# Kernel tuning notes

Hardware: AMD Instinct MI355X
Metric: run time of the kernel (lower is better)

The kernel has to match this reference:

```python
import jax, jax.numpy as jnp
import numpy as np

EPS = 1e-5

def _ln(x, g, b):
    mu = jnp.mean(x, axis=-1, keepdims=True)
    var = jnp.mean(jnp.square(x - mu), axis=-1, keepdims=True)
    return (x - mu) * jax.lax.rsqrt(var + EPS) * g + b


def setup_inputs() -> dict:
    key = jax.random.key(0)
    ks = jax.random.split(key, 16)
    B, T, D, H = 8, 4096, 512, 1024
    s_d = 1.0 / np.sqrt(D)
    s_h = 1.0 / np.sqrt(H)
    return {
        "x": jax.random.normal(ks[0], (B, T, D), dtype=jnp.float32),
        "gamma": jnp.ones((D,), jnp.float32),
        "beta": jnp.zeros((D,), jnp.float32),
        "Wq": jax.random.uniform(ks[1], (D, H), jnp.float32, -s_d, s_d),
        "bq": jax.random.uniform(ks[2], (H,), jnp.float32, -s_d, s_d),
        "Wk": jax.random.uniform(ks[3], (D, H), jnp.float32, -s_d, s_d),
        "bk": jax.random.uniform(ks[4], (H,), jnp.float32, -s_d, s_d),
        "Wv": jax.random.uniform(ks[5], (D, H), jnp.float32, -s_d, s_d),
        "bv": jax.random.uniform(ks[6], (H,), jnp.float32, -s_d, s_d),
        "wbias": jax.random.uniform(ks[7], (H,), jnp.float32, 0.0, 1.0),
        "Wo": jax.random.uniform(ks[8], (H, D), jnp.float32, -s_h, s_h),
        "bo": jax.random.uniform(ks[9], (D,), jnp.float32, -s_h, s_h),
        "W1": jax.random.uniform(ks[10], (D, H), jnp.float32, -s_d, s_d),
        "b1": jax.random.uniform(ks[11], (H,), jnp.float32, -s_d, s_d),
        "W2": jax.random.uniform(ks[12], (H, D), jnp.float32, -s_h, s_h),
        "b2": jax.random.uniform(ks[13], (D,), jnp.float32, -s_h, s_h),
    }


def reference(x, gamma, beta, Wq, bq, Wk, bk, Wv, bv, wbias, Wo, bo, W1, b1, W2, b2):
    # --- pre-LN ---
    x1 = _ln(x, gamma, beta)                      # [B,T,D]
    # --- AFTFull attention (NOTE: sums over BATCH dim 0, as in original repo) ---
    Q = jnp.einsum('btd,dh->bth', x1, Wq) + bq    # [B,T,H]
    K = jnp.einsum('btd,dh->bth', x1, Wk) + bk
    V = jnp.einsum('btd,dh->bth', x1, Wv) + bv
    Q_sig = jax.nn.sigmoid(Q)
    numer = jnp.exp(K + wbias)                    # [B,T,H]
    denom = jnp.sum(numer, axis=0)                # [T,H]
    weighted = jnp.sum(numer * V, axis=0) / denom # [T,H]
    Yt = Q_sig * weighted                         # [B,T,H] (broadcast)
    Yt = jnp.einsum('bth,hd->btd', Yt, Wo) + bo   # [B,T,D]
    x2 = Yt + x1                                  # residual (dropout = identity, eval)
    # --- second LN (same params, as in original) + MLP ---
    x3 = _ln(x2, gamma, beta)
    h = jax.nn.gelu(jnp.einsum('btd,dh->bth', x3, W1) + b1, approximate=False)
    m = jnp.einsum('bth,hd->btd', h, W2) + b2
    # original: out = dropout(m) + m  ==  2*m at eval (no residual to x2)
    return m + m
```

## Files before the change

kernel.cpp:

```cpp
#include <hip/hip_runtime.h>
#include <hip/hip_bf16.h>
#include <cstdint>

using u16 = unsigned short;
using u32 = unsigned int;

typedef __bf16 bf16x8 __attribute__((ext_vector_type(8)));
typedef float  f32x4  __attribute__((ext_vector_type(4)));

#define DEV static __device__ __forceinline__

DEV float bf2f(u16 u){ union { u32 u; float f; } c; c.u = ((u32)u) << 16; return c.f; }

DEV u16 f2bf(float f){
  __bf16 h = (__bf16)f;
  return __builtin_bit_cast(u16, h);
}

DEV float fast_rcp(float x){ return __builtin_amdgcn_rcpf(x); }

DEV void async16(const u16* g, u16* l){
  __builtin_amdgcn_global_load_lds((const __attribute__((address_space(1))) u32*)g,
                                   (__attribute__((address_space(3))) u32*)l,
                                   16, 0, 0);
}

__global__ __launch_bounds__(256)
void transpose_all(const float* __restrict__ W0, const float* __restrict__ W1,
                   const float* __restrict__ W2, const float* __restrict__ W3,
                   const float* __restrict__ W4, const float* __restrict__ W5,
                   u16* __restrict__ T0, u16* __restrict__ T1, u16* __restrict__ T2,
                   u16* __restrict__ T3, u16* __restrict__ T4, u16* __restrict__ T5){
  const int z = blockIdx.z;
  const float* W; u16* WT; int R, C;
  switch (z){
    case 0:  W = W0; WT = T0; R = 512;  C = 1024; break;
    case 1:  W = W1; WT = T1; R = 512;  C = 1024; break;
    case 2:  W = W2; WT = T2; R = 512;  C = 1024; break;
    case 3:  W = W3; WT = T3; R = 1024; C = 512;  break;
    case 4:  W = W4; WT = T4; R = 512;  C = 1024; break;
    default: W = W5; WT = T5; R = 1024; C = 512;  break;
  }
  const int c0 = blockIdx.x * 32, r0 = blockIdx.y * 32;
  if (c0 >= C || r0 >= R) return;
  __shared__ float tile[32][33];
  const int tx = threadIdx.x, ty = threadIdx.y;
  #pragma unroll
  for (int j = 0; j < 4; ++j)
    tile[ty + j*8][tx] = W[(size_t)(r0 + ty + j*8) * C + (c0 + tx)];
  __syncthreads();
  #pragma unroll
  for (int j = 0; j < 4; ++j)
    WT[(size_t)(c0 + ty + j*8) * R + (r0 + tx)] = f2bf(tile[tx][ty + j*8]);
}

template<bool BF16IN>
__global__ __launch_bounds__(256)
void ln_kernel(const void* __restrict__ xin, const float* __restrict__ gamma,
               const float* __restrict__ beta, u16* __restrict__ xout){
  const int wid = threadIdx.x >> 6;
  const int lane = threadIdx.x & 63;
  const size_t row = (size_t)blockIdx.x * 4 + wid;
  const int d0 = lane * 8;
  float v[8];
  if constexpr (BF16IN){
    const u16* xp = (const u16*)xin + row * 512 + d0;
    uint4 p = *(const uint4*)xp;
    const u16* s = (const u16*)&p;
    #pragma unroll
    for (int i = 0; i < 8; ++i) v[i] = bf2f(s[i]);
  } else {
    const float* xp = (const float*)xin + row * 512 + d0;
    float4 p0 = *(const float4*)xp;
    float4 p1 = *(const float4*)(xp + 4);
    v[0]=p0.x; v[1]=p0.y; v[2]=p0.z; v[3]=p0.w;
    v[4]=p1.x; v[5]=p1.y; v[6]=p1.z; v[7]=p1.w;
  }
  float s = 0.f, sq = 0.f;
  #pragma unroll
  for (int i = 0; i < 8; ++i){ s += v[i]; sq += v[i]*v[i]; }
  #pragma unroll
  for (int o = 32; o >= 1; o >>= 1){ s += __shfl_xor(s, o); sq += __shfl_xor(sq, o); }
  const float mu  = s * (1.0f/512.0f);
  const float var = sq * (1.0f/512.0f) - mu*mu;
  const float rstd = rsqrtf(var + 1e-5f);
  const float4 g0 = *(const float4*)(gamma + d0);
  const float4 g1 = *(const float4*)(gamma + d0 + 4);
  const float4 b0 = *(const float4*)(beta + d0);
  const float4 b1 = *(const float4*)(beta + d0 + 4);
  const float* gp = (const float*)&g0;
  float gg[8] = {g0.x,g0.y,g0.z,g0.w,g1.x,g1.y,g1.z,g1.w};
  float bb[8] = {b0.x,b0.y,b0.z,b0.w,b1.x,b1.y,b1.z,b1.w};
  (void)gp;
  u16 o8[8];
  #pragma unroll
  for (int i = 0; i < 8; ++i)
    o8[i] = f2bf((v[i]-mu)*rstd*gg[i] + bb[i]);
  *(uint4*)(xout + row*512 + d0) = *(const uint4*)o8;
}

__global__ __launch_bounds__(256)
void aft_fused(const u16* __restrict__ numer, const u16* __restrict__ V,
               const u16* __restrict__ qs, u16* __restrict__ yt){
  const size_t TH = (size_t)4096 * 1024;
  const size_t i8 = ((size_t)blockIdx.x * 256 + threadIdx.x) * 8;
  float den[8], ws[8];
  #pragma unroll
  for (int j = 0; j < 8; ++j){ den[j] = 0.f; ws[j] = 0.f; }
  #pragma unroll
  for (int b = 0; b < 8; ++b){
    uint4 pn = *(const uint4*)(numer + b*TH + i8);
    uint4 pv = *(const uint4*)(V     + b*TH + i8);
    const u16* n = (const u16*)&pn;
    const u16* v = (const u16*)&pv;
    #pragma unroll
    for (int j = 0; j < 8; ++j){ float nf = bf2f(n[j]); den[j] += nf; ws[j] += nf * bf2f(v[j]); }
  }
  float w[8];
  #pragma unroll
  for (int j = 0; j < 8; ++j) w[j] = ws[j] * fast_rcp(den[j]);
  #pragma unroll
  for (int b = 0; b < 8; ++b){
    uint4 pq = *(const uint4*)(qs + b*TH + i8);
    const u16* q = (const u16*)&pq;
    u16 o[8];
    #pragma unroll
    for (int j = 0; j < 8; ++j) o[j] = f2bf(bf2f(q[j]) * w[j]);
    *(uint4*)(yt + b*TH + i8) = *(const uint4*)o;
  }
}

template<int EPI, int KC>
__global__ __launch_bounds__(256, 3)
void gemm128(const u16* __restrict__ A, const u16* __restrict__ Bt, int nTiles,
             const float* __restrict__ bias0, const float* __restrict__ wbias,
             u16* __restrict__ out0, u16* __restrict__ out1, u16* __restrict__ out2,
             const float* __restrict__ bias1, const float* __restrict__ bias2,
             const u16* __restrict__ resid, float* __restrict__ outf){
  __shared__ u16 ldsA[128*64];
  __shared__ u16 ldsB[128*64];
  const int tid  = threadIdx.x;
  const int wid  = tid >> 6;
  const int lane = tid & 63;
  const int quad = lane >> 4;
  const int lr   = lane & 15;

  const int lin = blockIdx.x;
  const int GS  = 16 * nTiles;
  const int g   = lin / GS;
  const int rem = lin - g * GS;
  const int tileM = (g * 16 + (rem & 15)) * 128;
  const int tileN = (rem >> 4) * 128;

  const int wmBase = (wid & 1) * 64;
  const int wnBase = (wid >> 1) * 64;

  f32x4 acc[4][4] = {};

  int srow[4], scb[4];
  #pragma unroll
  for (int r = 0; r < 4; ++r){
    const int off = r*4096 + wid*1024 + lane*16;
    srow[r] = off >> 7;
    scb[r]  = ((off >> 4) & 7) ^ (srow[r] & 7);
  }
  const u16* aSrc[4]; const u16* bSrc[4];
  #pragma unroll
  for (int r = 0; r < 4; ++r){
    aSrc[r] = A  + (size_t)(tileM + srow[r]) * KC + scb[r]*8;
    bSrc[r] = Bt + (size_t)(tileN + srow[r]) * KC + scb[r]*8;
  }

  int aOff[2][4], bOff[2][4];
  #pragma unroll
  for (int s = 0; s < 2; ++s)
    #pragma unroll
    for (int i = 0; i < 4; ++i){
      const int m = wmBase + i*16 + lr;
      const int n = wnBase + i*16 + lr;
      aOff[s][i] = m*128 + (((s*4 + quad) ^ (m & 7)) * 16);
      bOff[s][i] = n*128 + (((s*4 + quad) ^ (n & 7)) * 16);
    }

  #pragma unroll
  for (int kt = 0; kt < KC; kt += 64){
    #pragma unroll
    for (int r = 0; r < 4; ++r){
      async16(aSrc[r] + kt, (u16*)((char*)ldsA + r*4096 + wid*1024));
      async16(bSrc[r] + kt, (u16*)((char*)ldsB + r*4096 + wid*1024));
    }
    __syncthreads();
    #pragma unroll
    for (int s = 0; s < 2; ++s){
      bf16x8 ar[4], br[4];
      #pragma unroll
      for (int i = 0; i < 4; ++i) ar[i] = *(const bf16x8*)((const char*)ldsA + aOff[s][i]);
      #pragma unroll
      for (int i = 0; i < 4; ++i) br[i] = *(const bf16x8*)((const char*)ldsB + bOff[s][i]);
      #pragma unroll
      for (int i = 0; i < 4; ++i)
        #pragma unroll
        for (int j = 0; j < 4; ++j)
          acc[i][j] = __builtin_amdgcn_mfma_f32_16x16x32_bf16(br[j], ar[i], acc[i][j], 0, 0, 0);
    }
    __syncthreads();
  }

  if (EPI == 3){
    #pragma unroll
    for (int j = 0; j < 4; ++j){
      const int colb = tileN + wnBase + j*16 + quad*4;
      const float4 bvv = *(const float4*)(bias0 + colb);
      #pragma unroll
      for (int i = 0; i < 4; ++i){
        const int row = tileM + wmBase + i*16 + lr;
        float4 o;
        #pragma unroll
        for (int r = 0; r < 4; ++r)
          ((float*)&o)[r] = 2.0f * (acc[i][j][r] + ((const float*)&bvv)[r]);
        *(float4*)(outf + (size_t)row * 512 + colb) = o;
      }
    }
    return;
  }

  u16* eb = ldsA + wid * 1152;
  const int mat = (EPI == 0) ? (tileN >> 10) : 0;
  const float* biasP = bias0;
  u16* outP = out0;
  int ldO = 1024, cb0 = tileN + wnBase;
  if (EPI == 0){
    biasP = (mat==0) ? bias0 : (mat==1) ? bias1 : bias2;
    outP  = (mat==0) ? out0  : (mat==1) ? out1  : out2;
    cb0   = (tileN & 1023) + wnBase;
  } else if (EPI == 1){
    ldO = 512;
  }

  #pragma unroll
  for (int i = 0; i < 4; ++i){
    const int row = tileM + wmBase + i*16 + lr;
    #pragma unroll
    for (int j = 0; j < 4; ++j){
      const int cl = j*16 + quad*4;
      const float4 bvv = *(const float4*)(biasP + cb0 + cl);
      u16 o[4];
      if (EPI == 0){
        float4 wbv = {0,0,0,0};
        if (mat == 1) wbv = *(const float4*)(wbias + cb0 + cl);
        #pragma unroll
        for (int r = 0; r < 4; ++r){
          float v = acc[i][j][r] + ((const float*)&bvv)[r];
          if (mat == 0)      v = fast_rcp(1.0f + __expf(-v));
          else if (mat == 1) v = __expf(v + ((const float*)&wbv)[r]);
          o[r] = f2bf(v);
        }
      } else if (EPI == 1){
        uint2 pr = *(const uint2*)(resid + (size_t)row * 512 + cb0 + cl);
        const u16* rp = (const u16*)&pr;
        #pragma unroll
        for (int r = 0; r < 4; ++r)
          o[r] = f2bf(acc[i][j][r] + ((const float*)&bvv)[r] + bf2f(rp[r]));
      } else {
        #pragma unroll
        for (int r = 0; r < 4; ++r){
          float v = acc[i][j][r] + ((const float*)&bvv)[r];
          float u2 = 2.0f * v * (0.7978845608f + 0.0356774081f * v * v);
          float t  = 1.0f - 2.0f * fast_rcp(1.0f + __expf(u2));
          o[r] = f2bf(0.5f * v * (1.0f + t));
        }
      }
      *(uint2*)(eb + lr*72 + cl) = *(const uint2*)o;
    }
    __asm__ volatile("s_waitcnt lgkmcnt(0)" ::: "memory");
    uint4 p0 = *(const uint4*)(eb + lr*72 + quad*16);
    uint4 p1 = *(const uint4*)(eb + lr*72 + quad*16 + 8);
    __asm__ volatile("s_waitcnt lgkmcnt(0)" ::: "memory");
    u16* gp = outP + (size_t)row * ldO + cb0 + quad*16;
    *(uint4*)gp = p0;
    *(uint4*)(gp + 8) = p1;
  }
}

extern "C" void kernel_launch(void* const* d_in, const int* in_sizes, int n_in,
                              void* d_out, int out_size, void* d_ws, size_t ws_size,
                              hipStream_t stream) {
  const float* x     = (const float*)d_in[0];
  const float* gamma = (const float*)d_in[1];
  const float* beta  = (const float*)d_in[2];
  const float* Wq    = (const float*)d_in[3];
  const float* bq    = (const float*)d_in[4];
  const float* Wk    = (const float*)d_in[5];
  const float* bk    = (const float*)d_in[6];
  const float* Wv    = (const float*)d_in[7];
  const float* bv    = (const float*)d_in[8];
  const float* wbias = (const float*)d_in[9];
  const float* Wo    = (const float*)d_in[10];
  const float* bo    = (const float*)d_in[11];
  const float* W1    = (const float*)d_in[12];
  const float* b1    = (const float*)d_in[13];
  const float* W2    = (const float*)d_in[14];
  const float* b2    = (const float*)d_in[15];
  float* out = (float*)d_out;

  char* w = (char*)d_ws;
  const size_t MB = 1ull << 20;
  u16* WqkvT = (u16*)(w + 0*MB);
  u16* WoT   = (u16*)(w + 3*MB);
  u16* W1T   = (u16*)(w + 4*MB);
  u16* W2T   = (u16*)(w + 5*MB);
  u16* x1b   = (u16*)(w + 6*MB);
  u16* Qs    = (u16*)(w + 38*MB);
  u16* Nu    = (u16*)(w + 102*MB);
  u16* Vb    = (u16*)(w + 166*MB);
  u16* Yt    = Nu;
  u16* x2b   = Vb;
  u16* x3b   = (u16*)(w + 198*MB);
  u16* hb    = Qs;

  transpose_all<<<dim3(32, 32, 6), dim3(32, 8), 0, stream>>>(
      Wq, Wk, Wv, Wo, W1, W2,
      WqkvT, WqkvT + 1024*512, WqkvT + 2*1024*512, WoT, W1T, W2T);

  ln_kernel<false><<<8192, 256, 0, stream>>>(x, gamma, beta, x1b);

  gemm128<0, 512><<<256*24, 256, 0, stream>>>(x1b, WqkvT, 24,
      bq, wbias, Qs, Nu, Vb, bk, bv, nullptr, nullptr);

  aft_fused<<<2048, 256, 0, stream>>>(Nu, Vb, Qs, Yt);

  gemm128<1, 1024><<<256*4, 256, 0, stream>>>(Yt, WoT, 4,
      bo, nullptr, x2b, nullptr, nullptr, nullptr, nullptr, x1b, nullptr);

  ln_kernel<true><<<8192, 256, 0, stream>>>(x2b, gamma, beta, x3b);

  gemm128<2, 512><<<256*8, 256, 0, stream>>>(x3b, W1T, 8,
      b1, nullptr, hb, nullptr, nullptr, nullptr, nullptr, nullptr, nullptr);

  gemm128<3, 1024><<<256*4, 256, 0, stream>>>(hb, W2T, 4,
      b2, nullptr, nullptr, nullptr, nullptr, nullptr, nullptr, nullptr, out);
}
```

Baseline: 486.7 us.

## Replace 128x128 GEMM with 256x256 ping-pong pipelined 8-wave GEMM

```diff
diff --git a/kernel.cpp b/kernel.cpp
--- a/kernel.cpp
+++ b/kernel.cpp
@@ -24,6 +24,11 @@
                                    (__attribute__((address_space(3))) u32*)l,
                                    16, 0, 0);
 }
+
+#define BARRIER() __builtin_amdgcn_s_barrier()
+#define LGKM0() do { __asm__ volatile("s_waitcnt lgkmcnt(0)" ::: "memory"); \
+                     __builtin_amdgcn_sched_barrier(0); } while (0)
+#define VMCNT(n) __asm__ volatile("s_waitcnt vmcnt(" #n ")" ::: "memory")
 
 __global__ __launch_bounds__(256)
 void transpose_all(const float* __restrict__ W0, const float* __restrict__ W1,
@@ -88,10 +93,8 @@
   const float4 g1 = *(const float4*)(gamma + d0 + 4);
   const float4 b0 = *(const float4*)(beta + d0);
   const float4 b1 = *(const float4*)(beta + d0 + 4);
-  const float* gp = (const float*)&g0;
   float gg[8] = {g0.x,g0.y,g0.z,g0.w,g1.x,g1.y,g1.z,g1.w};
   float bb[8] = {b0.x,b0.y,b0.z,b0.w,b1.x,b1.y,b1.z,b1.w};
-  (void)gp;
   u16 o8[8];
   #pragma unroll
   for (int i = 0; i < 8; ++i)
@@ -131,118 +134,177 @@
 }
 
 template<int EPI, int KC>
-__global__ __launch_bounds__(256, 3)
-void gemm128(const u16* __restrict__ A, const u16* __restrict__ Bt, int nTiles,
+__global__ __launch_bounds__(512, 2)
+void gemm256(const u16* __restrict__ A, const u16* __restrict__ Bt,
              const float* __restrict__ bias0, const float* __restrict__ wbias,
              u16* __restrict__ out0, u16* __restrict__ out1, u16* __restrict__ out2,
              const float* __restrict__ bias1, const float* __restrict__ bias2,
              const u16* __restrict__ resid, float* __restrict__ outf){
-  __shared__ u16 ldsA[128*64];
-  __shared__ u16 ldsB[128*64];
+  constexpr int NK = KC / 64;
+  __shared__ __align__(16) char smem[65536];
+
   const int tid  = threadIdx.x;
   const int wid  = tid >> 6;
   const int lane = tid & 63;
   const int quad = lane >> 4;
   const int lr   = lane & 15;
-
-  const int lin = blockIdx.x;
-  const int GS  = 16 * nTiles;
-  const int g   = lin / GS;
-  const int rem = lin - g * GS;
-  const int tileM = (g * 16 + (rem & 15)) * 128;
-  const int tileN = (rem >> 4) * 128;
-
-  const int wmBase = (wid & 1) * 64;
-  const int wnBase = (wid >> 1) * 64;
-
-  f32x4 acc[4][4] = {};
-
-  int srow[4], scb[4];
-  #pragma unroll
-  for (int r = 0; r < 4; ++r){
-    const int off = r*4096 + wid*1024 + lane*16;
-    srow[r] = off >> 7;
-    scb[r]  = ((off >> 4) & 7) ^ (srow[r] & 7);
-  }
-  const u16* aSrc[4]; const u16* bSrc[4];
-  #pragma unroll
-  for (int r = 0; r < 4; ++r){
-    aSrc[r] = A  + (size_t)(tileM + srow[r]) * KC + scb[r]*8;
-    bSrc[r] = Bt + (size_t)(tileN + srow[r]) * KC + scb[r]*8;
-  }
-
-  int aOff[2][4], bOff[2][4];
-  #pragma unroll
-  for (int s = 0; s < 2; ++s)
+  const int wm   = wid & 1;
+  const int wn   = wid >> 1;
+
+  const int nwg = gridDim.x;
+  const int wg  = (blockIdx.x & 7) * (nwg >> 3) + (blockIdx.x >> 3);
+  const int tileM = (wg & 127) * 256;
+  const int tileN = (wg >> 7) * 256;
+
+  const u16* sA[2][2]; const u16* sB[2][2];
+  {
+    const int off0 = wid*1024 + lane*16;
+    #pragma unroll
+    for (int r = 0; r < 2; ++r){
+      const int off = r*8192 + off0;
+      const int rr  = off >> 7;
+      const int g   = (((off >> 4) & 7) ^ (rr & 7)) * 8;
+      #pragma unroll
+      for (int h = 0; h < 2; ++h){
+        sA[h][r] = A  + (size_t)(tileM + (rr>>6)*128 + h*64 + (rr&63)) * KC + g;
+        sB[h][r] = Bt + (size_t)(tileN + (rr>>5)*64  + h*32 + (rr&31)) * KC + g;
+      }
+    }
+  }
+  auto stA = [&](int h, int kt){
+    char* d = smem + h*16384 + wid*1024;
+    async16(sA[h][0] + kt, (u16*)d);
+    async16(sA[h][1] + kt, (u16*)(d + 8192));
+  };
+  auto stB = [&](int h, int kt){
+    char* d = smem + 32768 + h*16384 + wid*1024;
+    async16(sB[h][0] + kt, (u16*)d);
+    async16(sB[h][1] + kt, (u16*)(d + 8192));
+  };
+
+  const int cO0  = ((quad)     ^ (lr & 7)) * 16;
+  const int cO1  = ((quad ^ 4) ^ (lr & 7)) * 16;
+  const int aRow = (wm*64 + lr) * 128;
+  const int bRow = (wn*32 + lr) * 128;
+
+  bf16x8 ar[4][2], br0[2][2], br1[2][2];
+  f32x4 acc[2][2][4][2] = {};
+
+  auto ldA = [&](int mh){
     #pragma unroll
     for (int i = 0; i < 4; ++i){
-      const int m = wmBase + i*16 + lr;
-      const int n = wnBase + i*16 + lr;
-      aOff[s][i] = m*128 + (((s*4 + quad) ^ (m & 7)) * 16);
-      bOff[s][i] = n*128 + (((s*4 + quad) ^ (n & 7)) * 16);
+      ar[i][0] = *(const bf16x8*)(smem + mh*16384 + aRow + i*2048 + cO0);
+      ar[i][1] = *(const bf16x8*)(smem + mh*16384 + aRow + i*2048 + cO1);
     }
-
-  #pragma unroll
-  for (int kt = 0; kt < KC; kt += 64){
-    #pragma unroll
-    for (int r = 0; r < 4; ++r){
-      async16(aSrc[r] + kt, (u16*)((char*)ldsA + r*4096 + wid*1024));
-      async16(bSrc[r] + kt, (u16*)((char*)ldsB + r*4096 + wid*1024));
+  };
+  auto ldB = [&](int nh, bf16x8 (&br)[2][2]){
+    #pragma unroll
+    for (int j = 0; j < 2; ++j){
+      br[j][0] = *(const bf16x8*)(smem + 32768 + nh*16384 + bRow + j*2048 + cO0);
+      br[j][1] = *(const bf16x8*)(smem + 32768 + nh*16384 + bRow + j*2048 + cO1);
     }
-    __syncthreads();
-    #pragma unroll
-    for (int s = 0; s < 2; ++s){
-      bf16x8 ar[4], br[4];
+  };
+  auto MF = [&](int mh, int nh, bf16x8 (&br)[2][2]){
+    __builtin_amdgcn_s_setprio(1);
+    #pragma unroll
+    for (int i = 0; i < 4; ++i)
       #pragma unroll
-      for (int i = 0; i < 4; ++i) ar[i] = *(const bf16x8*)((const char*)ldsA + aOff[s][i]);
+      for (int j = 0; j < 2; ++j){
+        acc[mh][nh][i][j] = __builtin_amdgcn_mfma_f32_16x16x32_bf16(br[j][0], ar[i][0], acc[mh][nh][i][j], 0, 0, 0);
+        acc[mh][nh][i][j] = __builtin_amdgcn_mfma_f32_16x16x32_bf16(br[j][1], ar[i][1], acc[mh][nh][i][j], 0, 0, 0);
+      }
+    __builtin_amdgcn_s_setprio(0);
+  };
+
+  stA(0, 0); stB(0, 0); stB(1, 0); stA(1, 0);
+  VMCNT(4);
+  BARRIER();
+
+  #pragma unroll 1
+  for (int t = 0; t < NK-1; ++t){
+    const int kt = (t+1)*64;
+    ldA(0); ldB(0, br0);
+    BARRIER(); LGKM0();
+    MF(0, 0, br0);
+    VMCNT(2);
+    BARRIER();
+    ldB(1, br1);
+    stA(0, kt); stB(0, kt);
+    BARRIER(); LGKM0();
+    MF(0, 1, br1);
+    VMCNT(4);
+    BARRIER();
+    ldA(1);
+    stB(1, kt);
+    BARRIER(); LGKM0();
+    MF(1, 1, br1);
+    BARRIER();
+    stA(1, kt);
+    MF(1, 0, br0);
+    VMCNT(4);
+    BARRIER();
+  }
+  ldA(0); ldB(0, br0);
+  BARRIER(); LGKM0();
+  MF(0, 0, br0);
+  VMCNT(2);
+  BARRIER();
+  ldB(1, br1);
+  BARRIER(); LGKM0();
+  MF(0, 1, br1);
+  VMCNT(0);
+  BARRIER();
+  ldA(1);
+  BARRIER(); LGKM0();
+  MF(1, 1, br1);
+  BARRIER();
+  MF(1, 0, br0);
+
+  if (EPI == 3){
+    #pragma unroll
+    for (int mh = 0; mh < 2; ++mh)
+    #pragma unroll
+    for (int i = 0; i < 4; ++i){
+      const int row = tileM + wm*128 + mh*64 + i*16 + lr;
       #pragma unroll
-      for (int i = 0; i < 4; ++i) br[i] = *(const bf16x8*)((const char*)ldsB + bOff[s][i]);
+      for (int nh = 0; nh < 2; ++nh)
       #pragma unroll
-      for (int i = 0; i < 4; ++i)
-        #pragma unroll
-        for (int j = 0; j < 4; ++j)
-          acc[i][j] = __builtin_amdgcn_mfma_f32_16x16x32_bf16(br[j], ar[i], acc[i][j], 0, 0, 0);
-    }
-    __syncthreads();
-  }
-
-  if (EPI == 3){
-    #pragma unroll
-    for (int j = 0; j < 4; ++j){
-      const int colb = tileN + wnBase + j*16 + quad*4;
-      const float4 bvv = *(const float4*)(bias0 + colb);
-      #pragma unroll
-      for (int i = 0; i < 4; ++i){
-        const int row = tileM + wmBase + i*16 + lr;
+      for (int j = 0; j < 2; ++j){
+        const int colb = tileN + wn*64 + nh*32 + j*16 + quad*4;
+        const float4 bvv = *(const float4*)(bias0 + colb);
         float4 o;
         #pragma unroll
         for (int r = 0; r < 4; ++r)
-          ((float*)&o)[r] = 2.0f * (acc[i][j][r] + ((const float*)&bvv)[r]);
+          ((float*)&o)[r] = 2.0f * (acc[mh][nh][i][j][r] + ((const float*)&bvv)[r]);
         *(float4*)(outf + (size_t)row * 512 + colb) = o;
       }
     }
     return;
   }
 
-  u16* eb = ldsA + wid * 1152;
+  char* eb = smem + wid * 2304;
   const int mat = (EPI == 0) ? (tileN >> 10) : 0;
   const float* biasP = bias0;
   u16* outP = out0;
-  int ldO = 1024, cb0 = tileN + wnBase;
+  int ldO = 1024, cb0 = tileN + wn*64;
   if (EPI == 0){
     biasP = (mat==0) ? bias0 : (mat==1) ? bias1 : bias2;
     outP  = (mat==0) ? out0  : (mat==1) ? out1  : out2;
-    cb0   = (tileN & 1023) + wnBase;
+    cb0   = (tileN & 1023) + wn*64;
   } else if (EPI == 1){
     ldO = 512;
   }
 
   #pragma unroll
+  for (int mh = 0; mh < 2; ++mh)
+  #pragma unroll
   for (int i = 0; i < 4; ++i){
-    const int row = tileM + wmBase + i*16 + lr;
-    #pragma unroll
-    for (int j = 0; j < 4; ++j){
-      const int cl = j*16 + quad*4;
+    const int row = tileM + wm*128 + mh*64 + i*16 + lr;
+    #pragma unroll
+    for (int nh = 0; nh < 2; ++nh)
+    #pragma unroll
+    for (int j = 0; j < 2; ++j){
+      const int cl = (nh*2 + j)*16 + quad*4;
       const float4 bvv = *(const float4*)(biasP + cb0 + cl);
       u16 o[4];
       if (EPI == 0){
@@ -250,7 +312,7 @@
         if (mat == 1) wbv = *(const float4*)(wbias + cb0 + cl);
         #pragma unroll
         for (int r = 0; r < 4; ++r){
-          float v = acc[i][j][r] + ((const float*)&bvv)[r];
+          float v = acc[mh][nh][i][j][r] + ((const float*)&bvv)[r];
           if (mat == 0)      v = fast_rcp(1.0f + __expf(-v));
           else if (mat == 1) v = __expf(v + ((const float*)&wbv)[r]);
           o[r] = f2bf(v);
@@ -260,21 +322,21 @@
         const u16* rp = (const u16*)&pr;
         #pragma unroll
         for (int r = 0; r < 4; ++r)
-          o[r] = f2bf(acc[i][j][r] + ((const float*)&bvv)[r] + bf2f(rp[r]));
+          o[r] = f2bf(acc[mh][nh][i][j][r] + ((const float*)&bvv)[r] + bf2f(rp[r]));
       } else {
         #pragma unroll
         for (int r = 0; r < 4; ++r){
-          float v = acc[i][j][r] + ((const float*)&bvv)[r];
+          float v  = acc[mh][nh][i][j][r] + ((const float*)&bvv)[r];
           float u2 = 2.0f * v * (0.7978845608f + 0.0356774081f * v * v);
-          float t  = 1.0f - 2.0f * fast_rcp(1.0f + __expf(u2));
-          o[r] = f2bf(0.5f * v * (1.0f + t));
+          float tg = 1.0f - 2.0f * fast_rcp(1.0f + __expf(u2));
+          o[r] = f2bf(0.5f * v * (1.0f + tg));
         }
       }
-      *(uint2*)(eb + lr*72 + cl) = *(const uint2*)o;
+      *(uint2*)(eb + lr*144 + cl*2) = *(const uint2*)o;
     }
     __asm__ volatile("s_waitcnt lgkmcnt(0)" ::: "memory");
-    uint4 p0 = *(const uint4*)(eb + lr*72 + quad*16);
-    uint4 p1 = *(const uint4*)(eb + lr*72 + quad*16 + 8);
+    uint4 p0 = *(const uint4*)(eb + lr*144 + quad*32);
+    uint4 p1 = *(const uint4*)(eb + lr*144 + quad*32 + 16);
     __asm__ volatile("s_waitcnt lgkmcnt(0)" ::: "memory");
     u16* gp = outP + (size_t)row * ldO + cb0 + quad*16;
     *(uint4*)gp = p0;
@@ -324,19 +386,19 @@
 
   ln_kernel<false><<<8192, 256, 0, stream>>>(x, gamma, beta, x1b);
 
-  gemm128<0, 512><<<256*24, 256, 0, stream>>>(x1b, WqkvT, 24,
+  gemm256<0, 512><<<1536, 512, 0, stream>>>(x1b, WqkvT,
       bq, wbias, Qs, Nu, Vb, bk, bv, nullptr, nullptr);
 
   aft_fused<<<2048, 256, 0, stream>>>(Nu, Vb, Qs, Yt);
 
-  gemm128<1, 1024><<<256*4, 256, 0, stream>>>(Yt, WoT, 4,
+  gemm256<1, 1024><<<256, 512, 0, stream>>>(Yt, WoT,
       bo, nullptr, x2b, nullptr, nullptr, nullptr, nullptr, x1b, nullptr);
 
   ln_kernel<true><<<8192, 256, 0, stream>>>(x2b, gamma, beta, x3b);
 
-  gemm128<2, 512><<<256*8, 256, 0, stream>>>(x3b, W1T, 8,
+  gemm256<2, 512><<<512, 512, 0, stream>>>(x3b, W1T,
       b1, nullptr, hb, nullptr, nullptr, nullptr, nullptr, nullptr, nullptr);
 
-  gemm128<3, 1024><<<256*4, 256, 0, stream>>>(hb, W2T, 4,
+  gemm256<3, 1024><<<256, 512, 0, stream>>>(hb, W2T,
       b2, nullptr, nullptr, nullptr, nullptr, nullptr, nullptr, nullptr, out);
 }
```

Measured after the change: 484.0 us. About the same (-0.6%).
